# Kernel optimization log

Hardware: AMD Instinct MI355X
Metric: run time of the kernel (lower is better)

Reference implementation:

```python
import jax, jax.numpy as jnp
import numpy as np
from jax.scipy.special import logsumexp

B, T, D = 16, 512, 768
S, H, O = 4, 48, 48
EMISS_W = 0.5  # args.emiss_nn_weight


def setup_inputs() -> dict:
    key = jax.random.key(0)
    ks = jax.random.split(key, 6)
    emb = jax.random.normal(ks[0], (B, T, D), jnp.float32)
    # obs must be valid per-source distributions over n_obs (log is taken)
    obs = jax.nn.softmax(2.0 * jax.random.normal(ks[1], (B, T, S, O), jnp.float32), axis=-1)
    # default prior init: priors = 0.001, priors[0] = 1, param = log(priors)
    p = jnp.full((H,), 0.001, jnp.float32).at[0].set(1.0)
    state_priors = jnp.log(p)
    unnorm_trans = jax.random.normal(ks[2], (H, H), jnp.float32)
    unnorm_emiss = jnp.zeros((S, H, O), jnp.float32)
    # xavier_uniform with relu gain for the per-source emission Linears
    bound = np.sqrt(2.0) * np.sqrt(6.0 / (D + H * O))
    W_emiss = jax.random.uniform(ks[3], (S, H * O, D), jnp.float32, -bound, bound)
    b_emiss = jnp.zeros((S, H * O), jnp.float32)
    seq_lengths = jax.random.randint(ks[4], (B,), T // 2, T + 1).astype(jnp.int32)
    seq_lengths = seq_lengths.at[0].set(T)  # max length == T
    return dict(emb=emb, obs=obs, state_priors=state_priors, unnorm_trans=unnorm_trans,
                unnorm_emiss=unnorm_emiss, W_emiss=W_emiss, b_emiss=b_emiss,
                seq_lengths=seq_lengths)


def _lognorm(x):
    return x - logsumexp(x, axis=-1, keepdims=True)


def reference(emb, obs, state_priors, unnorm_trans, unnorm_emiss, W_emiss, b_emiss, seq_lengths):
    lp = jax.nn.log_softmax(state_priors)                 # [H]
    log_trans = jax.nn.log_softmax(unnorm_trans, axis=-1)  # [H,H] (constant over b,t)
    emiss = jax.nn.softmax(unnorm_emiss, axis=-1)          # [S,H,O]

    # neural emissions: per-source Linear(d_emb -> H*O), softmax over O
    logits = jnp.einsum('btd,sod->btso', emb, W_emiss) + b_emiss  # [B,T,S,H*O]
    nn_emiss = jax.nn.softmax(logits.reshape(B, T, S, H, O), axis=-1)
    # (nn_trans is computed by NeuralModule in the original but discarded)

    log_emiss = jnp.log((1.0 - EMISS_W) * emiss[None, None] + EMISS_W * nn_emiss)  # [B,T,S,H,O]
    # log_matmul over obs axis, then sum over sources -> [B,T,H]
    lep = logsumexp(log_emiss + jnp.log(obs)[:, :, :, None, :], axis=-1).sum(axis=2)

    # forward recursion (normalized each step)
    a0 = _lognorm(lp + lep[:, 0])                          # [B,H]

    def fstep(a_prev, lep_t):
        a = _lognorm(lep_t + logsumexp(a_prev[:, :, None] + log_trans[None], axis=1))
        return a, a

    _, alphas = jax.lax.scan(fstep, a0, jnp.swapaxes(lep[:, 1:], 0, 1))
    log_alpha = jnp.concatenate([a0[:, None], jnp.swapaxes(alphas, 0, 1)], axis=1)  # [B,T,H]

    # backward recursion: beta[t] = logsumexp_j(trans[i,j] + lep[t,j] + beta[t+1,j])
    bT = jnp.zeros((B, H), lep.dtype)

    def bstep(b_next, lep_t):
        b = logsumexp(log_trans[None] + (lep_t + b_next)[:, None, :], axis=2)
        return b, b

    _, betas = jax.lax.scan(bstep, bT, jnp.swapaxes(lep[:, :T - 1], 0, 1), reverse=True)
    log_beta = jnp.concatenate([jnp.swapaxes(betas, 0, 1), bT[:, None]], axis=1)  # [B,T,H]
    # per-example roll by (length - T) along time, as in the original
    log_beta = jax.vmap(lambda b, s: jnp.roll(b, s, axis=0))(log_beta, seq_lengths - T)

    log_gamma = _lognorm(log_alpha + log_beta)             # [B,T,H]

    # xi_t = trans + alpha[t-1] (outer-sum) (lep[t] + beta[t]),  t = 1..T-1
    xi = (log_trans[None, None]
          + log_alpha[:, :-1, :, None]
          + (lep[:, 1:] + log_beta[:, 1:])[:, :, None, :])  # [B,T-1,H,H]
    xi = xi - logsumexp(xi, axis=(-2, -1), keepdims=True)

    log_prior = jnp.mean(jnp.sum(jnp.exp(log_gamma[:, 0]) * lp, axis=-1))

    tran_terms = jnp.sum(jnp.exp(xi) * log_trans[None, None], axis=(-2, -1))  # [B,T-1]
    mask_tr = (jnp.arange(T - 1)[None] < (seq_lengths - 1)[:, None]).astype(lep.dtype)
    log_tran = jnp.mean(jnp.sum(tran_terms * mask_tr, axis=1))

    emis_terms = jnp.sum(jnp.exp(log_gamma) * lep, axis=-1)  # [B,T]
    mask_em = (jnp.arange(T)[None] < seq_lengths[:, None]).astype(lep.dtype)
    log_emis = jnp.mean(jnp.sum(emis_terms * mask_em, axis=1))

    return log_prior + log_tran + log_emis
```

## Files before the change

kernel.cpp:

```cpp
#include <hip/hip_runtime.h>
#include <math.h>

namespace {

constexpr int Bn = 16, Tn = 512, Dn = 768, Sn = 4, Hn = 48, On = 48;
constexpr int Mn = Bn * Tn;
constexpr int Gn = Sn * Hn;
constexpr int Nn = Gn * On;
constexpr float EMISS_W = 0.5f;

constexpr size_t OFF_LP   = 0;
constexpr size_t OFF_LT   = 64;
constexpr size_t OFF_PT   = OFF_LT + Hn*Hn;
constexpr size_t OFF_EM   = OFF_PT + Hn*Hn;
constexpr size_t OFF_LEPP = OFF_EM + (size_t)Sn*Hn*On;
constexpr size_t OFF_LA   = OFF_LEPP + (size_t)Mn*Gn;
constexpr size_t OFF_LB   = OFF_LA + (size_t)Mn*Hn;
constexpr size_t OFF_RED  = OFF_LB + (size_t)Mn*Hn;
constexpr size_t FLOATS_END = OFF_RED + (size_t)Mn;

typedef __attribute__((ext_vector_type(8))) short short8;
typedef __attribute__((ext_vector_type(4))) float f32x4;

__device__ inline float waveSum(float v){
#pragma unroll
  for (int o = 32; o; o >>= 1) v += __shfl_xor(v, o);
  return v;
}

__device__ inline unsigned short f2bf(float f){
  unsigned int u = __float_as_uint(f);
  u += 0x7FFFu + ((u >> 16) & 1u);
  return (unsigned short)(u >> 16);
}

__device__ inline void gload_lds16(const void* g, void* l){
  __builtin_amdgcn_global_load_lds(
      (const __attribute__((address_space(1))) void*)g,
      (__attribute__((address_space(3))) void*)l, 16, 0, 0);
}

__global__ void convprep_kernel(const float* __restrict__ srcA, unsigned short* __restrict__ dstA,
                                int n4a,
                                const float* __restrict__ srcB, unsigned short* __restrict__ dstB,
                                int n4b,
                                const float* __restrict__ sp, const float* __restrict__ ut,
                                const float* __restrict__ ue, float* __restrict__ ws,
                                int nconv){
  const int tid = threadIdx.x;
  if ((int)blockIdx.x == nconv){
    float m = -INFINITY;
    for (int h = 0; h < Hn; ++h) m = fmaxf(m, sp[h]);
    float s = 0.f;
    for (int h = 0; h < Hn; ++h) s += __expf(sp[h] - m);
    float lse = m + __logf(s);
    if (tid < Hn) ws[OFF_LP + tid] = sp[tid] - lse;
    if (tid < Hn){
      const float* row = ut + tid * Hn;
      float mm = -INFINITY;
      for (int j = 0; j < Hn; ++j) mm = fmaxf(mm, row[j]);
      float ss = 0.f;
      for (int j = 0; j < Hn; ++j) ss += __expf(row[j] - mm);
      float l = mm + __logf(ss);
      for (int j = 0; j < Hn; ++j){
        float v = row[j] - l;
        ws[OFF_LT + tid*Hn + j] = v;
        ws[OFF_PT + tid*Hn + j] = __expf(v);
      }
    }
    for (int r = tid; r < Sn*Hn; r += blockDim.x){
      const float* row = ue + (size_t)r * On;
      float mm = -INFINITY;
      for (int o = 0; o < On; ++o) mm = fmaxf(mm, row[o]);
      float ss = 0.f;
      for (int o = 0; o < On; ++o) ss += __expf(row[o] - mm);
      float inv = 1.f/ss;
      for (int o = 0; o < On; ++o) ws[OFF_EM + (size_t)r*On + o] = __expf(row[o]-mm)*inv;
    }
    return;
  }
  int i = blockIdx.x * blockDim.x + tid;
  const float* s2; unsigned short* d; int k;
  if (i < n4a){ s2 = srcA; d = dstA; k = i; }
  else { k = i - n4a; if (k >= n4b) return; s2 = srcB; d = dstB; }
  float4 v = ((const float4*)s2)[k];
  ushort4 r;
  r.x = f2bf(v.x); r.y = f2bf(v.y); r.z = f2bf(v.z); r.w = f2bf(v.w);
  ((ushort4*)d)[k] = r;
}

constexpr int BM = 256, BN = 192, BK = 64;
constexpr int NKT = Dn / BK;

#define GEMM_BAR()  asm volatile("s_barrier" ::: "memory")
#define GEMM_LGKM() do { asm volatile("s_waitcnt lgkmcnt(0)" ::: "memory"); \
                         __builtin_amdgcn_sched_barrier(0); } while (0)

__global__ __launch_bounds__(512, 2) void gemm_lep_kernel(
    const unsigned short* __restrict__ embB, const unsigned short* __restrict__ WB,
    const float* __restrict__ bm, const float* __restrict__ obs,
    float* __restrict__ ws){
  __shared__ __align__(16) char smem[114688];
  __shared__ float bias_s[192], em_s[192];
  const int tid = threadIdx.x, lane = tid & 63, w = tid >> 6;
  const int bid = blockIdx.y * (Mn/BM) + blockIdx.x;
  const int swz = (bid & 7) * 192 + (bid >> 3);
  const int m0 = (swz & 31) * BM;
  const int by = swz >> 5;
  const int N0 = by * BN;
  if (tid < 192){
    bias_s[tid] = bm[N0 + tid];
    em_s[tid]   = ws[OFF_EM + N0 + tid];
  }
  const int wm = w & 1, wn = w >> 1;
  const int lm = lane & 15, q = lane >> 4;
  const int key = lm & 7;
  const int srow = lane >> 3, spc = lane & 7;
  const int aoff0 = (q ^ key) << 4;
  const int aoff1 = ((4 + q) ^ key) << 4;

  f32x4 acc[8][3];
#pragma unroll
  for (int i = 0; i < 8; ++i)
#pragma unroll
    for (int j = 0; j < 3; ++j) acc[i][j] = (f32x4){0.f,0.f,0.f,0.f};

  auto stageA = [&](int kt, int i){
    const int idx = w*4 + i;
    const int row = idx*8 + srow;
    const int lc  = spc ^ (row & 7);
    gload_lds16(embB + (size_t)(m0+row)*Dn + kt*BK + lc*8,
                smem + ((kt & 1) << 15) + idx*1024);
  };
  auto stageB = [&](int kt, int i){
    const int idx = w*3 + i;
    const int row = idx*8 + srow;
    const int lc  = spc ^ (row & 7);
    gload_lds16(WB + (size_t)(N0+row)*Dn + kt*BK + lc*8,
                smem + 65536 + (kt & 1)*24576 + idx*1024);
  };

#pragma unroll
  for (int i = 0; i < 4; ++i) stageA(0, i);
#pragma unroll
  for (int i = 0; i < 3; ++i) stageB(0, i);
  asm volatile("s_waitcnt vmcnt(0)" ::: "memory");
  GEMM_BAR();

  for (int kt = 0; kt < NKT; ++kt){
    const char* Ab = smem + ((kt & 1) << 15);
    const char* Bb = smem + 65536 + (kt & 1)*24576;
    const int pf = kt + 1;
    const bool dopf = pf < NKT;
    short8 af[4], bf[3];

#pragma unroll
    for (int j = 0; j < 3; ++j)
      bf[j] = *(const short8*)(Bb + (wn*48 + j*16 + lm)*128 + aoff0);
#pragma unroll
    for (int i = 0; i < 4; ++i)
      af[i] = *(const short8*)(Ab + (wm*128 + i*16 + lm)*128 + aoff0);
    if (dopf){ stageA(pf, 0); stageA(pf, 1); stageB(pf, 0); }
    GEMM_BAR(); GEMM_LGKM();
    __builtin_amdgcn_s_setprio(1);
#pragma unroll
    for (int i = 0; i < 4; ++i)
#pragma unroll
      for (int j = 0; j < 3; ++j)
        acc[i][j] = __builtin_amdgcn_mfma_f32_16x16x32_bf16(af[i], bf[j], acc[i][j], 0, 0, 0);
    __builtin_amdgcn_s_setprio(0);
    GEMM_BAR();

#pragma unroll
    for (int i = 0; i < 4; ++i)
      af[i] = *(const short8*)(Ab + (wm*128 + (4+i)*16 + lm)*128 + aoff0);
    if (dopf){ stageA(pf, 2); stageA(pf, 3); stageB(pf, 1); }
    GEMM_BAR(); GEMM_LGKM();
    __builtin_amdgcn_s_setprio(1);
#pragma unroll
    for (int i = 0; i < 4; ++i)
#pragma unroll
      for (int j = 0; j < 3; ++j)
        acc[4+i][j] = __builtin_amdgcn_mfma_f32_16x16x32_bf16(af[i], bf[j], acc[4+i][j], 0, 0, 0);
    __builtin_amdgcn_s_setprio(0);
    GEMM_BAR();

#pragma unroll
    for (int j = 0; j < 3; ++j)
      bf[j] = *(const short8*)(Bb + (wn*48 + j*16 + lm)*128 + aoff1);
#pragma unroll
    for (int i = 0; i < 4; ++i)
      af[i] = *(const short8*)(Ab + (wm*128 + i*16 + lm)*128 + aoff1);
    if (dopf){ stageB(pf, 2); }
    GEMM_BAR(); GEMM_LGKM();
    __builtin_amdgcn_s_setprio(1);
#pragma unroll
    for (int i = 0; i < 4; ++i)
#pragma unroll
      for (int j = 0; j < 3; ++j)
        acc[i][j] = __builtin_amdgcn_mfma_f32_16x16x32_bf16(af[i], bf[j], acc[i][j], 0, 0, 0);
    __builtin_amdgcn_s_setprio(0);
    GEMM_BAR();

#pragma unroll
    for (int i = 0; i < 4; ++i)
      af[i] = *(const short8*)(Ab + (wm*128 + (4+i)*16 + lm)*128 + aoff1);
    GEMM_BAR(); GEMM_LGKM();
    __builtin_amdgcn_s_setprio(1);
#pragma unroll
    for (int i = 0; i < 4; ++i)
#pragma unroll
      for (int j = 0; j < 3; ++j)
        acc[4+i][j] = __builtin_amdgcn_mfma_f32_16x16x32_bf16(af[i], bf[j], acc[4+i][j], 0, 0, 0);
    __builtin_amdgcn_s_setprio(0);
    asm volatile("s_waitcnt vmcnt(0)" ::: "memory");
    GEMM_BAR();
  }

  float* Cp = (float*)smem;
#pragma unroll
  for (int h = 0; h < 2; ++h){
    if (h) __syncthreads();
#pragma unroll
    for (int i = 0; i < 4; ++i)
#pragma unroll
      for (int j = 0; j < 3; ++j){
        const int col = wn*48 + j*16 + lm;
#pragma unroll
        for (int r = 0; r < 4; ++r){
          const int rowl = wm*64 + i*16 + q*4 + r;
          Cp[rowl*193 + col] = acc[h*4+i][j][r];
        }
      }
    __syncthreads();
    {
      const int rowl = tid >> 2, grp = tid & 3;
      const int trow = (rowl >> 6)*128 + h*64 + (rowl & 63);
      const int m = m0 + trow;
      const int g = by*4 + grp;
      const int s2 = g / Hn;
      const float* crow = Cp + rowl*193 + grp*48;
      const float* ob   = obs + ((size_t)m*Sn + s2)*On;
      const float* bi   = bias_s + grp*48;
      const float* em   = em_s + grp*48;
      float Z = 0.f, pd = 0.f, eo = 0.f;
#pragma unroll
      for (int o = 0; o < On; ++o){
        float e = __expf(crow[o] + bi[o]);
        float obv = ob[o];
        Z += e;
        pd = fmaf(e, obv, pd);
        eo = fmaf(em[o], obv, eo);
      }
      ws[OFF_LEPP + (size_t)m*Gn + g] = __logf((1.f-EMISS_W)*eo + EMISS_W*(pd/Z));
    }
  }
}

constexpr int FBW = 24;
constexpr int FBL = 16;

__global__ __launch_bounds__(64) void fb_kernel(float* __restrict__ ws){
  __shared__ __align__(16) float ldsE[(FBW+FBL)*48];
  __shared__ __align__(16) float ring[2][64];
  const int lane = threadIdx.x;
  const int c    = blockIdx.x;
  const int b    = blockIdx.y;
  const bool fwd = blockIdx.z == 0;
  const bool act = lane < Hn;
  const int t0 = c*FBL, te = t0 + FBL - 1;

  float pt[Hn];
#pragma unroll
  for (int i = 0; i < Hn; ++i)
    pt[i] = act ? (fwd ? ws[OFF_PT + i*Hn + lane] : ws[OFF_PT + lane*Hn + i]) : 0.f;

  int row_lo, nrows, sA, sZ;
  bool exact;
  if (fwd){
    sA = t0 - FBW;
    exact = (sA < 1);
    row_lo = exact ? 0 : sA;
    if (exact) sA = 1;
    sZ = te;
    nrows = te - row_lo + 1;
  } else {
    int th = te + 1 + FBW;
    exact = (th > Tn - 2);
    sA = exact ? Tn - 2 : th - 1;
    sZ = t0;
    row_lo = t0;
    nrows = sA - t0 + 1;
  }

  {
    const float* src = ws + OFF_LEPP + ((size_t)b*Tn + row_lo)*Gn;
    int n4 = nrows * (Hn/4);
    for (int i = lane; i < n4; i += 64){
      int r = i / (Hn/4), h4 = i - r*(Hn/4);
      const float* p = src + (size_t)r*Gn + h4*4;
      float4 a = *(const float4*)(p);
      float4 b2 = *(const float4*)(p + Hn);
      float4 c2 = *(const float4*)(p + 2*Hn);
      float4 d2 = *(const float4*)(p + 3*Hn);
      float4 e;
      e.x = __expf(a.x + b2.x + c2.x + d2.x);
      e.y = __expf(a.y + b2.y + c2.y + d2.y);
      e.z = __expf(a.z + b2.z + c2.z + d2.z);
      e.w = __expf(a.w + b2.w + c2.w + d2.w);
      ((float4*)ldsE)[i] = e;
    }
  }
  __syncthreads();

  if (fwd){
    const size_t laF = OFF_LA + (size_t)b * Tn * Hn;
    float v;
    if (exact){
      v = act ? __expf(ws[OFF_LP + lane]) * ldsE[lane] : 0.f;
      if (c == 0 && act) ws[laF + lane] = v;
    } else {
      v = act ? 1.f : 0.f;
    }
    if (act) ring[0][lane] = v;
    __syncthreads();
    int cur = 0;
    for (int t = sA; t <= sZ; ++t){
      float S = waveSum(v);
      const float* rp = ring[cur];
      float s0=0.f,s1=0.f,s2=0.f,s3=0.f;
#pragma unroll
      for (int i = 0; i < Hn; i += 4){
        float4 a = *(const float4*)(rp + i);
        s0 = fmaf(a.x, pt[i+0], s0); s1 = fmaf(a.y, pt[i+1], s1);
        s2 = fmaf(a.z, pt[i+2], s2); s3 = fmaf(a.w, pt[i+3], s3);
      }
      float sd = (s0+s1)+(s2+s3);
      float e = act ? ldsE[(t - row_lo)*Hn + lane] : 0.f;
      float vn = act ? e * sd * (1.f/S) : 0.f;
      cur ^= 1;
      if (act) ring[cur][lane] = vn;
      __syncthreads();
      if (act && t >= t0) ws[laF + (size_t)t*Hn + lane] = vn;
      v = vn;
    }
  } else {
    const size_t lbF = OFF_LB + (size_t)b * Tn * Hn;
    float v = act ? 1.f : 0.f;
    if (exact && c == (Tn/FBL - 1) && act) ws[lbF + (size_t)(Tn-1)*Hn + lane] = 1.f;
    int cur = 0;
    for (int t = sA; t >= sZ; --t){
      float e = act ? ldsE[(t - row_lo)*Hn + lane] : 0.f;
      float wv = e * v;
      if (act) ring[cur][lane] = wv;
      float S = waveSum(wv);
      __syncthreads();
      const float* rp = ring[cur];
      float s0=0.f,s1=0.f,s2=0.f,s3=0.f;
#pragma unroll
      for (int j = 0; j < Hn; j += 4){
        float4 a = *(const float4*)(rp + j);
        s0 = fmaf(a.x, pt[j+0], s0); s1 = fmaf(a.y, pt[j+1], s1);
        s2 = fmaf(a.z, pt[j+2], s2); s3 = fmaf(a.w, pt[j+3], s3);
      }
      float vn = act ? ((s0+s1)+(s2+s3)) * (1.f/S) : 0.f;
      cur ^= 1;
      if (act && t <= te) ws[lbF + (size_t)t*Hn + lane] = vn;
      v = vn;
    }
  }
}

__global__ __launch_bounds__(256) void gamma_xi_kernel(
    const float* __restrict__ ws_c, float* __restrict__ ws,
    const int* __restrict__ seq_len){
  __shared__ float y_s[Hn], lap_s[Hn];
  __shared__ float red[8];
  const int tid = threadIdx.x;
  const int bid = blockIdx.x;
  const int b = bid >> 9, t = bid & (Tn-1);
  const int len = seq_len[b];
  int tb = t + (Tn - len); if (tb >= Tn) tb -= Tn;
  const size_t bt = (size_t)b*Tn + t;
  float lep = 0.f;
  if (tid < Hn){
    const float* lpp = ws_c + OFF_LEPP + bt*Gn + tid;
    lep = lpp[0] + lpp[Hn] + lpp[2*Hn] + lpp[3*Hn];
    float lb  = ws_c[OFF_LB + ((size_t)b*Tn + tb)*Hn + tid];
    y_s[tid] = __expf(lep) * lb;
    if (t >= 1) lap_s[tid] = ws_c[OFF_LA + (bt-1)*Hn + tid];
  }
  float emis_term = 0.f, prior_term = 0.f;
  if (tid < 64){
    int h = (tid < Hn) ? tid : 0;
    float la  = ws_c[OFF_LA + bt*Hn + h];
    float lb  = ws_c[OFF_LB + ((size_t)b*Tn + tb)*Hn + h];
    float lp  = ws_c[OFF_LP + h];
    float wgt = (tid < Hn) ? la*lb : 0.f;
    float Z = waveSum(wgt);
    float inv = 1.f / Z;
    emis_term  = waveSum(wgt * lep) * inv;
    prior_term = waveSum(wgt * lp) * inv;
  }
  __syncthreads();
  float tran_term = 0.f;
  if (t >= 1){
    float se = 0.f, st = 0.f;
#pragma unroll
    for (int k=0;k<9;++k){
      int e = tid + k*256;
      int i = e / Hn, j = e - i*Hn;
      float e2 = ws_c[OFF_PT + e] * lap_s[i] * y_s[j];
      se += e2;
      st = fmaf(e2, ws_c[OFF_LT + e], st);
    }
    se = waveSum(se);
    st = waveSum(st);
    const int wid = tid >> 6;
    if ((tid & 63) == 0){ red[wid] = se; red[4+wid] = st; }
    __syncthreads();
    if (tid == 0){
      float SE = red[0]+red[1]+red[2]+red[3];
      float ST = red[4]+red[5]+red[6]+red[7];
      tran_term = ST / SE;
    }
  }
  if (tid == 0){
    float tot = 0.f;
    if (t < len)            tot += emis_term;
    if (t == 0)             tot += prior_term;
    if (t >= 1 && t < len)  tot += tran_term;
    ws[OFF_RED + bid] = tot;
  }
}

__global__ __launch_bounds__(256) void sum_kernel(const float* __restrict__ ws,
                                                  float* __restrict__ out){
  __shared__ float red[4];
  const int tid = threadIdx.x;
  float s = 0.f;
  for (int i = tid; i < Mn; i += 256) s += ws[OFF_RED + i];
  s = waveSum(s);
  if ((tid & 63) == 0) red[tid >> 6] = s;
  __syncthreads();
  if (tid == 0) out[0] = (red[0]+red[1]+red[2]+red[3]) * (1.f / Bn);
}

}

extern "C" void kernel_launch(void* const* d_in, const int* in_sizes, int n_in,
                              void* d_out, int out_size, void* d_ws, size_t ws_size,
                              hipStream_t stream){
  const float* emb = (const float*)d_in[0];
  const float* obs = (const float*)d_in[1];
  const float* sp  = (const float*)d_in[2];
  const float* ut  = (const float*)d_in[3];
  const float* ue  = (const float*)d_in[4];
  const float* Wm  = (const float*)d_in[5];
  const float* bm  = (const float*)d_in[6];
  const int*   sl  = (const int*)d_in[7];
  float* ws  = (float*)d_ws;
  float* out = (float*)d_out;
  (void)in_sizes; (void)n_in; (void)ws_size; (void)out_size;

  unsigned short* embB = (unsigned short*)(ws + FLOATS_END);
  unsigned short* WB   = embB + (size_t)Mn * Dn;

  const int n4a = Mn*Dn/4, n4b = Nn*Dn/4;
  const int nconv = (n4a + n4b + 255)/256;
  convprep_kernel<<<nconv + 1, 256, 0, stream>>>(emb, embB, n4a, Wm, WB, n4b,
                                                 sp, ut, ue, ws, nconv);
  gemm_lep_kernel<<<dim3(Mn/BM, Nn/BN), 512, 0, stream>>>(embB, WB, bm, obs, ws);
  fb_kernel<<<dim3(Tn/FBL, Bn, 2), 64, 0, stream>>>(ws);
  gamma_xi_kernel<<<Bn*Tn, 256, 0, stream>>>(ws, ws, sl);
  sum_kernel<<<1, 256, 0, stream>>>(ws, out);
}
```

Before: 313.2 us.

## Deepen GEMM prefetch to two k-tiles, batch LDS reads, remap tiles per XCD

The bf16 GEMM main loop now prefetches two k-tiles ahead while still using two LDS buffers. Each half of the current tile is loaded into registers before its LDS slot is overwritten by the next-next tile. Fragment loads for both k-halves are batched, which cuts barriers per iteration from four phases to two and uses vmcnt(7) waits instead of draining everything. Block-to-tile mapping is also rewritten so each XCD covers a compact 8x24 sub-grid, aiming for better L2 reuse. In exchange, fragment register use doubles, which with 96 accumulators under launch_bounds(512,2) risks spills or lower occupancy.

Measured after the change: 288.8 us. 1.08x faster.

```diff
diff --git a/kernel.cpp b/kernel.cpp
--- a/kernel.cpp
+++ b/kernel.cpp
@@ -104,9 +104,11 @@
   __shared__ float bias_s[192], em_s[192];
   const int tid = threadIdx.x, lane = tid & 63, w = tid >> 6;
   const int bid = blockIdx.y * (Mn/BM) + blockIdx.x;
-  const int swz = (bid & 7) * 192 + (bid >> 3);
-  const int m0 = (swz & 31) * BM;
-  const int by = swz >> 5;
+  const int xcd = bid & 7, j_loc = bid >> 3;
+  const int xm = xcd & 3, xn = xcd >> 2;
+  const int mloc = j_loc & 7, nloc = j_loc >> 3;
+  const int m0 = (xm*8 + mloc) * BM;
+  const int by = xn*24 + nloc;
   const int N0 = by * BN;
   if (tid < 192){
     bias_s[tid] = bm[N0 + tid];
@@ -125,12 +127,12 @@
 #pragma unroll
     for (int j = 0; j < 3; ++j) acc[i][j] = (f32x4){0.f,0.f,0.f,0.f};
 
-  auto stageA = [&](int kt, int i){
-    const int idx = w*4 + i;
-    const int row = idx*8 + srow;
+  auto stageA2 = [&](int kt, int rb){
+    const int r0  = rb + w*8;
+    const int row = r0 + srow;
     const int lc  = spc ^ (row & 7);
     gload_lds16(embB + (size_t)(m0+row)*Dn + kt*BK + lc*8,
-                smem + ((kt & 1) << 15) + idx*1024);
+                smem + ((kt & 1) << 15) + r0*128);
   };
   auto stageB = [&](int kt, int i){
     const int idx = w*3 + i;
@@ -140,80 +142,75 @@
                 smem + 65536 + (kt & 1)*24576 + idx*1024);
   };
 
-#pragma unroll
-  for (int i = 0; i < 4; ++i) stageA(0, i);
-#pragma unroll
-  for (int i = 0; i < 3; ++i) stageB(0, i);
-  asm volatile("s_waitcnt vmcnt(0)" ::: "memory");
+  stageA2(0,0); stageA2(0,64); stageA2(0,128); stageA2(0,192);
+  stageB(0,0);  stageB(0,1);   stageB(0,2);
+  stageA2(1,0); stageA2(1,64); stageA2(1,128); stageA2(1,192);
+  stageB(1,0);  stageB(1,1);   stageB(1,2);
+  asm volatile("s_waitcnt vmcnt(7)" ::: "memory");
   GEMM_BAR();
 
   for (int kt = 0; kt < NKT; ++kt){
     const char* Ab = smem + ((kt & 1) << 15);
     const char* Bb = smem + 65536 + (kt & 1)*24576;
-    const int pf = kt + 1;
+    const int pf = kt + 2;
     const bool dopf = pf < NKT;
-    short8 af[4], bf[3];
-
-#pragma unroll
-    for (int j = 0; j < 3; ++j)
-      bf[j] = *(const short8*)(Bb + (wn*48 + j*16 + lm)*128 + aoff0);
+    short8 af0[4], af1[4], bf0[3], bf1[3];
+
+#pragma unroll
+    for (int j = 0; j < 3; ++j){
+      const char* bp = Bb + (wn*48 + j*16 + lm)*128;
+      bf0[j] = *(const short8*)(bp + aoff0);
+      bf1[j] = *(const short8*)(bp + aoff1);
+    }
+#pragma unroll
+    for (int i = 0; i < 4; ++i){
+      const char* ap = Ab + (wm*128 + i*16 + lm)*128;
+      af0[i] = *(const short8*)(ap + aoff0);
+      af1[i] = *(const short8*)(ap + aoff1);
+    }
+    GEMM_LGKM();
+    GEMM_BAR();
+    if (dopf){
+      stageA2(pf, 0); stageA2(pf, 128);
+      stageB(pf, 0); stageB(pf, 1); stageB(pf, 2);
+    }
+    __builtin_amdgcn_s_setprio(1);
 #pragma unroll
     for (int i = 0; i < 4; ++i)
-      af[i] = *(const short8*)(Ab + (wm*128 + i*16 + lm)*128 + aoff0);
-    if (dopf){ stageA(pf, 0); stageA(pf, 1); stageB(pf, 0); }
-    GEMM_BAR(); GEMM_LGKM();
+#pragma unroll
+      for (int j = 0; j < 3; ++j)
+        acc[i][j] = __builtin_amdgcn_mfma_f32_16x16x32_bf16(af0[i], bf0[j], acc[i][j], 0, 0, 0);
+#pragma unroll
+    for (int i = 0; i < 4; ++i)
+#pragma unroll
+      for (int j = 0; j < 3; ++j)
+        acc[i][j] = __builtin_amdgcn_mfma_f32_16x16x32_bf16(af1[i], bf1[j], acc[i][j], 0, 0, 0);
+    __builtin_amdgcn_s_setprio(0);
+
+#pragma unroll
+    for (int i = 0; i < 4; ++i){
+      const char* ap = Ab + (wm*128 + (4+i)*16 + lm)*128;
+      af0[i] = *(const short8*)(ap + aoff0);
+      af1[i] = *(const short8*)(ap + aoff1);
+    }
+    GEMM_LGKM();
+    GEMM_BAR();
+    if (dopf){ stageA2(pf, 64); stageA2(pf, 192); }
     __builtin_amdgcn_s_setprio(1);
 #pragma unroll
     for (int i = 0; i < 4; ++i)
 #pragma unroll
       for (int j = 0; j < 3; ++j)
-        acc[i][j] = __builtin_amdgcn_mfma_f32_16x16x32_bf16(af[i], bf[j], acc[i][j], 0, 0, 0);
+        acc[4+i][j] = __builtin_amdgcn_mfma_f32_16x16x32_bf16(af0[i], bf0[j], acc[4+i][j], 0, 0, 0);
+#pragma unroll
+    for (int i = 0; i < 4; ++i)
+#pragma unroll
+      for (int j = 0; j < 3; ++j)
+        acc[4+i][j] = __builtin_amdgcn_mfma_f32_16x16x32_bf16(af1[i], bf1[j], acc[4+i][j], 0, 0, 0);
     __builtin_amdgcn_s_setprio(0);
-    GEMM_BAR();
-
-#pragma unroll
-    for (int i = 0; i < 4; ++i)
-      af[i] = *(const short8*)(Ab + (wm*128 + (4+i)*16 + lm)*128 + aoff0);
-    if (dopf){ stageA(pf, 2); stageA(pf, 3); stageB(pf, 1); }
-    GEMM_BAR(); GEMM_LGKM();
-    __builtin_amdgcn_s_setprio(1);
-#pragma unroll
-    for (int i = 0; i < 4; ++i)
-#pragma unroll
-      for (int j = 0; j < 3; ++j)
-        acc[4+i][j] = __builtin_amdgcn_mfma_f32_16x16x32_bf16(af[i], bf[j], acc[4+i][j], 0, 0, 0);
-    __builtin_amdgcn_s_setprio(0);
-    GEMM_BAR();
-
-#pragma unroll
-    for (int j = 0; j < 3; ++j)
-      bf[j] = *(const short8*)(Bb + (wn*48 + j*16 + lm)*128 + aoff1);
-#pragma unroll
-    for (int i = 0; i < 4; ++i)
-      af[i] = *(const short8*)(Ab + (wm*128 + i*16 + lm)*128 + aoff1);
-    if (dopf){ stageB(pf, 2); }
-    GEMM_BAR(); GEMM_LGKM();
-    __builtin_amdgcn_s_setprio(1);
-#pragma unroll
-    for (int i = 0; i < 4; ++i)
-#pragma unroll
-      for (int j = 0; j < 3; ++j)
-        acc[i][j] = __builtin_amdgcn_mfma_f32_16x16x32_bf16(af[i], bf[j], acc[i][j], 0, 0, 0);
-    __builtin_amdgcn_s_setprio(0);
-    GEMM_BAR();
-
-#pragma unroll
-    for (int i = 0; i < 4; ++i)
-      af[i] = *(const short8*)(Ab + (wm*128 + (4+i)*16 + lm)*128 + aoff1);
-    GEMM_BAR(); GEMM_LGKM();
-    __builtin_amdgcn_s_setprio(1);
-#pragma unroll
-    for (int i = 0; i < 4; ++i)
-#pragma unroll
-      for (int j = 0; j < 3; ++j)
-        acc[4+i][j] = __builtin_amdgcn_mfma_f32_16x16x32_bf16(af[i], bf[j], acc[4+i][j], 0, 0, 0);
-    __builtin_amdgcn_s_setprio(0);
-    asm volatile("s_waitcnt vmcnt(0)" ::: "memory");
+
+    if (kt <= NKT-3)      asm volatile("s_waitcnt vmcnt(7)" ::: "memory");
+    else if (kt == NKT-2) asm volatile("s_waitcnt vmcnt(0)" ::: "memory");
     GEMM_BAR();
   }
 
```

## Retune GEMM block-to-XCD mapping, prefetch distribution, and drop sched barrier

Applied to the files above, without the earlier changes.

Changes the block swizzle so each XCD covers a 2D sub-grid of M and N tiles (8 M-tiles by 24 N-tiles), intended to improve L2 reuse of both operands per XCD. Redistributes next-tile A/B prefetch loads across the first three sub-phases and lays out A rows contiguously per wave, balancing global-load issue. Removes the sched_barrier after the LDS wait, letting the compiler reorder MFMAs and loads, which risks worse scheduling or hazards.

After: 299.5 us. -4.4%, faster.

```diff
diff --git a/kernel.cpp b/kernel.cpp
--- a/kernel.cpp
+++ b/kernel.cpp
@@ -93,8 +93,7 @@
 constexpr int NKT = Dn / BK;
 
 #define GEMM_BAR()  asm volatile("s_barrier" ::: "memory")
-#define GEMM_LGKM() do { asm volatile("s_waitcnt lgkmcnt(0)" ::: "memory"); \
-                         __builtin_amdgcn_sched_barrier(0); } while (0)
+#define GEMM_LGKM() asm volatile("s_waitcnt lgkmcnt(0)" ::: "memory")
 
 __global__ __launch_bounds__(512, 2) void gemm_lep_kernel(
     const unsigned short* __restrict__ embB, const unsigned short* __restrict__ WB,
@@ -104,9 +103,11 @@
   __shared__ float bias_s[192], em_s[192];
   const int tid = threadIdx.x, lane = tid & 63, w = tid >> 6;
   const int bid = blockIdx.y * (Mn/BM) + blockIdx.x;
-  const int swz = (bid & 7) * 192 + (bid >> 3);
-  const int m0 = (swz & 31) * BM;
-  const int by = swz >> 5;
+  const int xcd = bid & 7, j_loc = bid >> 3;
+  const int xm = xcd & 3, xn = xcd >> 2;
+  const int mloc = j_loc & 7, nloc = j_loc >> 3;
+  const int m0 = (xm*8 + mloc) * BM;
+  const int by = xn*24 + nloc;
   const int N0 = by * BN;
   if (tid < 192){
     bias_s[tid] = bm[N0 + tid];
@@ -125,12 +126,12 @@
 #pragma unroll
     for (int j = 0; j < 3; ++j) acc[i][j] = (f32x4){0.f,0.f,0.f,0.f};
 
-  auto stageA = [&](int kt, int i){
-    const int idx = w*4 + i;
-    const int row = idx*8 + srow;
+  auto stageA2 = [&](int kt, int rb){
+    const int r0  = rb + w*8;
+    const int row = r0 + srow;
     const int lc  = spc ^ (row & 7);
     gload_lds16(embB + (size_t)(m0+row)*Dn + kt*BK + lc*8,
-                smem + ((kt & 1) << 15) + idx*1024);
+                smem + ((kt & 1) << 15) + r0*128);
   };
   auto stageB = [&](int kt, int i){
     const int idx = w*3 + i;
@@ -140,10 +141,8 @@
                 smem + 65536 + (kt & 1)*24576 + idx*1024);
   };
 
-#pragma unroll
-  for (int i = 0; i < 4; ++i) stageA(0, i);
-#pragma unroll
-  for (int i = 0; i < 3; ++i) stageB(0, i);
+  stageA2(0,0); stageA2(0,64); stageA2(0,128); stageA2(0,192);
+  stageB(0,0);  stageB(0,1);   stageB(0,2);
   asm volatile("s_waitcnt vmcnt(0)" ::: "memory");
   GEMM_BAR();
 
@@ -160,8 +159,9 @@
 #pragma unroll
     for (int i = 0; i < 4; ++i)
       af[i] = *(const short8*)(Ab + (wm*128 + i*16 + lm)*128 + aoff0);
-    if (dopf){ stageA(pf, 0); stageA(pf, 1); stageB(pf, 0); }
-    GEMM_BAR(); GEMM_LGKM();
+    if (dopf){ stageA2(pf, 0); stageA2(pf, 64); }
+    GEMM_BAR();
+    GEMM_LGKM();
     __builtin_amdgcn_s_setprio(1);
 #pragma unroll
     for (int i = 0; i < 4; ++i)
@@ -174,8 +174,9 @@
 #pragma unroll
     for (int i = 0; i < 4; ++i)
       af[i] = *(const short8*)(Ab + (wm*128 + (4+i)*16 + lm)*128 + aoff0);
-    if (dopf){ stageA(pf, 2); stageA(pf, 3); stageB(pf, 1); }
-    GEMM_BAR(); GEMM_LGKM();
+    if (dopf){ stageA2(pf, 128); stageA2(pf, 192); stageB(pf, 0); }
+    GEMM_BAR();
+    GEMM_LGKM();
     __builtin_amdgcn_s_setprio(1);
 #pragma unroll
     for (int i = 0; i < 4; ++i)
@@ -191,8 +192,9 @@
 #pragma unroll
     for (int i = 0; i < 4; ++i)
       af[i] = *(const short8*)(Ab + (wm*128 + i*16 + lm)*128 + aoff1);
-    if (dopf){ stageB(pf, 2); }
-    GEMM_BAR(); GEMM_LGKM();
+    if (dopf){ stageB(pf, 1); stageB(pf, 2); }
+    GEMM_BAR();
+    GEMM_LGKM();
     __builtin_amdgcn_s_setprio(1);
 #pragma unroll
     for (int i = 0; i < 4; ++i)
@@ -205,7 +207,8 @@
 #pragma unroll
     for (int i = 0; i < 4; ++i)
       af[i] = *(const short8*)(Ab + (wm*128 + (4+i)*16 + lm)*128 + aoff1);
-    GEMM_BAR(); GEMM_LGKM();
+    GEMM_BAR();
+    GEMM_LGKM();
     __builtin_amdgcn_s_setprio(1);
 #pragma unroll
     for (int i = 0; i < 4; ++i)
```
